# Kernel tuning notes

Measured on AMD Instinct MI355X. Metric: run time of the kernel, lower is better.

## Reference

```python
import jax, jax.numpy as jnp
import numpy as np

V, D, T, B, H, L, FF = 32000, 1024, 1024, 2, 16, 2, 4096


def _ln(x, g, b, eps=1e-5):
    m = x.mean(-1, keepdims=True)
    v = ((x - m) ** 2).mean(-1, keepdims=True)
    return (x - m) * jax.lax.rsqrt(v + eps) * g + b


def setup_inputs() -> dict:
    key = jax.random.key(0)
    ks = jax.random.split(key, 16)
    s = 0.02  # init scale for stable softmax/logits
    return {
        "idx": jax.random.randint(ks[0], (B, T), 0, V),
        "targets": jax.random.randint(ks[1], (B, T), 0, V),
        "word_emb": jax.random.normal(ks[2], (V, D), jnp.float32) * s,
        "pos_emb": jax.random.normal(ks[3], (T, D), jnp.float32) * s,
        "ln1_g": jnp.ones((L, D), jnp.float32),
        "ln1_b": jnp.zeros((L, D), jnp.float32),
        "wq": jax.random.normal(ks[4], (L, D, D), jnp.float32) * s,
        "wk": jax.random.normal(ks[5], (L, D, D), jnp.float32) * s,
        "wv": jax.random.normal(ks[6], (L, D, D), jnp.float32) * s,
        "proj_w": jax.random.normal(ks[7], (L, D, D), jnp.float32) * s,
        "proj_b": jnp.zeros((L, D), jnp.float32),
        "ln2_g": jnp.ones((L, D), jnp.float32),
        "ln2_b": jnp.zeros((L, D), jnp.float32),
        "ff_w1": jax.random.normal(ks[8], (L, D, FF), jnp.float32) * s,
        "ff_b1": jnp.zeros((L, FF), jnp.float32),
        "ff_w2": jax.random.normal(ks[9], (L, FF, D), jnp.float32) * s,
        "ff_b2": jnp.zeros((L, D), jnp.float32),
        "lnf_g": jnp.ones((D,), jnp.float32),
        "lnf_b": jnp.zeros((D,), jnp.float32),
        "lm_w": jax.random.normal(ks[10], (D, V), jnp.float32) * s,
        "lm_b": jnp.zeros((V,), jnp.float32),
    }


def reference(word_emb, pos_emb, ln1_g, ln1_b, wq, wk, wv, proj_w, proj_b,
              ln2_g, ln2_b, ff_w1, ff_b1, ff_w2, ff_b2, lnf_g, lnf_b,
              lm_w, lm_b, idx, targets):
    b, t = idx.shape
    d = word_emb.shape[1]
    n_layer, n_head = wq.shape[0], H
    x = word_emb[idx] + pos_emb[:t]              # [B,T,D]
    causal = jnp.tril(jnp.ones((t, t), bool))
    maps = []
    for l in range(n_layer):
        h = _ln(x, ln1_g[l], ln1_b[l])
        q = (h @ wq[l]).reshape(b, t, n_head, -1)  # [B,T,H,hd]
        k = (h @ wk[l]).reshape(b, t, n_head, -1)
        v = (h @ wv[l]).reshape(b, t, n_head, -1)
        # NOTE: source scales by n_embd**-0.5 (full embedding dim), not head_size
        wei = jnp.einsum('bqhd,bkhd->bhqk', q, k) * (d ** -0.5)
        wei = jnp.where(causal, wei, -jnp.inf)
        wei = jax.nn.softmax(wei, axis=-1)        # [B,H,T,T]
        maps.append(wei)
        att = jnp.einsum('bhqk,bkhd->bqhd', wei, v).reshape(b, t, d)
        x = x + att @ proj_w[l] + proj_b[l]
        h2 = _ln(x, ln2_g[l], ln2_b[l])
        x = x + jax.nn.relu(h2 @ ff_w1[l] + ff_b1[l]) @ ff_w2[l] + ff_b2[l]
    x = _ln(x, lnf_g, lnf_b)
    logits = (x @ lm_w + lm_b).reshape(b * t, -1)  # [B*T, V]
    logp = jax.nn.log_softmax(logits, axis=-1)
    loss = -logp[jnp.arange(b * t), targets.reshape(-1)].mean()
    probs = jax.nn.log_softmax(x, axis=-1)         # source: LogSoftmax of final-LN x
    return (logits, loss, jnp.stack(maps), probs)
```

## Files before the change

### kernel.cpp

```cpp
#include <hip/hip_runtime.h>
#include <hip/hip_bf16.h>

#define VSZ 32000
#define DM  1024
#define TSEQ 1024
#define BB  2
#define HH  16
#define LL  2
#define FFD 4096
#define NTOK (BB*TSEQ)

static constexpr size_t LOGITS_OFF = 0;
static constexpr size_t LOSS_OFF   = (size_t)NTOK * VSZ;
static constexpr size_t MAPS_OFF   = LOSS_OFF + 1;
static constexpr size_t PROBS_OFF  = MAPS_OFF + (size_t)LL*BB*HH*TSEQ*TSEQ;

typedef __attribute__((ext_vector_type(8))) short bf8;
typedef __attribute__((ext_vector_type(4))) float f32x4;
typedef __attribute__((ext_vector_type(4))) short short4v;

__device__ __forceinline__ short f2bf(float f) {
  union { float f; unsigned u; } v; v.f = f;
  unsigned r = v.u + 0x7FFFu + ((v.u >> 16) & 1u);
  return (short)(r >> 16);
}

__device__ __forceinline__ void gload16(const void* g, void* l) {
  __builtin_amdgcn_global_load_lds(
      (const __attribute__((address_space(1))) void*)g,
      (__attribute__((address_space(3))) void*)l, 16, 0, 0);
}

__device__ __forceinline__ float block_sum256(float v, float* sh) {
#pragma unroll
  for (int off = 32; off; off >>= 1) v += __shfl_down(v, off);
  int wid = threadIdx.x >> 6, lane = threadIdx.x & 63;
  if (lane == 0) sh[wid] = v;
  __syncthreads();
  v = sh[0] + sh[1] + sh[2] + sh[3];
  __syncthreads();
  return v;
}
__device__ __forceinline__ float block_max256(float v, float* sh) {
#pragma unroll
  for (int off = 32; off; off >>= 1) v = fmaxf(v, __shfl_down(v, off));
  int wid = threadIdx.x >> 6, lane = threadIdx.x & 63;
  if (lane == 0) sh[wid] = v;
  __syncthreads();
  v = fmaxf(fmaxf(sh[0], sh[1]), fmaxf(sh[2], sh[3]));
  __syncthreads();
  return v;
}

static constexpr size_t PLW = (size_t)4 * DM * DM + (size_t)DM * FFD + (size_t)FFD * DM;
__global__ __launch_bounds__(256) void transpose_all(const float* __restrict__ wq,
    const float* __restrict__ wk, const float* __restrict__ wv,
    const float* __restrict__ proj_w, const float* __restrict__ ff_w1,
    const float* __restrict__ ff_w2, short* __restrict__ wt_base) {
  __shared__ float T[64][65];
  const int bid = blockIdx.x;
  const int l = bid / 3072, r = bid % 3072;
  short* qbase = wt_base + (size_t)l * PLW;
  const float* W; short* Wt; int K, N, tn, tk;
  if (r < 1024) {
    int s = r >> 8, rr = r & 255;
    W = (s == 0 ? wq : (s == 1 ? wk : (s == 2 ? wv : proj_w))) + (size_t)l * DM * DM;
    Wt = qbase + (size_t)s * DM * DM;
    K = DM; N = DM; tn = rr & 15; tk = rr >> 4;
  } else if (r < 2048) {
    int rr = r - 1024;
    W = ff_w1 + (size_t)l * DM * FFD; Wt = qbase + (size_t)4 * DM * DM;
    K = DM; N = FFD; tn = rr & 63; tk = rr >> 6;
  } else {
    int rr = r - 2048;
    W = ff_w2 + (size_t)l * FFD * DM; Wt = qbase + (size_t)4 * DM * DM + (size_t)DM * FFD;
    K = FFD; N = DM; tn = rr & 15; tk = rr >> 4;
  }
  const int n0 = tn * 64, k0 = tk * 64;
  const int tid = threadIdx.x;
  const int lr = tid >> 4, lc4 = (tid & 15) * 4;
#pragma unroll
  for (int p = 0; p < 4; ++p) {
    int k = lr + p * 16;
    float4 w = *(const float4*)&W[(size_t)(k0 + k) * N + n0 + lc4];
    T[k][lc4] = w.x; T[k][lc4+1] = w.y; T[k][lc4+2] = w.z; T[k][lc4+3] = w.w;
  }
  __syncthreads();
#pragma unroll
  for (int p = 0; p < 4; ++p) {
    int n = lr + p * 16;
    short4v s;
    s.x = f2bf(T[lc4  ][n]);
    s.y = f2bf(T[lc4+1][n]);
    s.z = f2bf(T[lc4+2][n]);
    s.w = f2bf(T[lc4+3][n]);
    *(short4v*)&Wt[(size_t)(n0 + n) * K + k0 + lc4] = s;
  }
}

__global__ __launch_bounds__(256) void transpose_cvt(const float* __restrict__ W,
    short* __restrict__ Wt, int K, int N) {
  __shared__ float T[64][65];
  const int n0 = blockIdx.x * 64, k0 = blockIdx.y * 64;
  const int tid = threadIdx.x;
  const int lr = tid >> 4, lc4 = (tid & 15) * 4;
#pragma unroll
  for (int p = 0; p < 4; ++p) {
    int k = lr + p * 16;
    float4 w = *(const float4*)&W[(size_t)(k0 + k) * N + n0 + lc4];
    T[k][lc4] = w.x; T[k][lc4+1] = w.y; T[k][lc4+2] = w.z; T[k][lc4+3] = w.w;
  }
  __syncthreads();
#pragma unroll
  for (int p = 0; p < 4; ++p) {
    int n = lr + p * 16;
    short4v s;
    s.x = f2bf(T[lc4  ][n]);
    s.y = f2bf(T[lc4+1][n]);
    s.z = f2bf(T[lc4+2][n]);
    s.w = f2bf(T[lc4+3][n]);
    *(short4v*)&Wt[(size_t)(n0 + n) * K + k0 + lc4] = s;
  }
}

__global__ __launch_bounds__(256) void embed_kernel(const int* __restrict__ idx,
    const float* __restrict__ we, const float* __restrict__ pe, float* __restrict__ x) {
  int i = blockIdx.x * 256 + threadIdx.x;
  int n = i >> 10;
  int d = i & 1023;
  int t = n & (TSEQ - 1);
  x[i] = we[(size_t)idx[n] * DM + d] + pe[(size_t)t * DM + d];
}

template<int ALSO_F32>
__global__ __launch_bounds__(256) void ln_bf(const float* __restrict__ in,
    const float* __restrict__ g, const float* __restrict__ b,
    short* __restrict__ outb, float* __restrict__ outf) {
  __shared__ float sh[4];
  int row = blockIdx.x, tid = threadIdx.x;
  const float* xr = in + (size_t)row * DM;
  float4 v = *(const float4*)&xr[tid * 4];
  float s  = v.x + v.y + v.z + v.w;
  float s2 = v.x*v.x + v.y*v.y + v.z*v.z + v.w*v.w;
  s  = block_sum256(s, sh);
  s2 = block_sum256(s2, sh);
  float mean = s * (1.0f / DM);
  float var  = s2 * (1.0f / DM) - mean * mean;
  float inv  = rsqrtf(var + 1e-5f);
  float4 gv = *(const float4*)&g[tid * 4];
  float4 bv = *(const float4*)&b[tid * 4];
  float4 o;
  o.x = (v.x - mean) * inv * gv.x + bv.x;
  o.y = (v.y - mean) * inv * gv.y + bv.y;
  o.z = (v.z - mean) * inv * gv.z + bv.z;
  o.w = (v.w - mean) * inv * gv.w + bv.w;
  short4v ob;
  ob.x = f2bf(o.x); ob.y = f2bf(o.y); ob.z = f2bf(o.z); ob.w = f2bf(o.w);
  *(short4v*)&outb[(size_t)row * DM + tid * 4] = ob;
  if (ALSO_F32)
    *(float4*)&outf[(size_t)row * DM + tid * 4] = o;
}

template<int BIAS, int RES, int RELU, int OUTBF>
__global__ __launch_bounds__(256) void gemm_bb(const short* __restrict__ A, int lda,
    const short* __restrict__ Bt, const float* __restrict__ bias,
    void* __restrict__ Cv, int M, int K, int Nn) {
  __shared__ short As[128 * 32];
  __shared__ short Bs[128 * 32];
  float* Cf = (float*)Cv;
  short* Cb = (short*)Cv;
  const int tid  = threadIdx.x;
  const int bm   = blockIdx.x * 128, bn = blockIdx.y * 128;
  const int lane = tid & 63, wid = tid >> 6;
  const int wr = wid >> 1, wc = wid & 1;
  const int lr = lane & 15, lg = lane >> 4;
  const int srow = lane >> 2;
  const int schunk = (lane & 3) * 8;

  f32x4 acc[4][4];
#pragma unroll
  for (int i = 0; i < 4; ++i)
#pragma unroll
    for (int j = 0; j < 4; ++j) acc[i][j] = (f32x4)0.f;

  for (int k0 = 0; k0 < K; k0 += 32) {
#pragma unroll
    for (int t = 0; t < 2; ++t) {
      const int issue = wid * 2 + t;
      const int row = issue * 16 + srow;
      gload16(&A[(size_t)(bm + row) * lda + k0 + schunk], &As[issue * 512]);
      gload16(&Bt[(size_t)(bn + row) * K  + k0 + schunk], &Bs[issue * 512]);
    }
    __syncthreads();
    bf8 af[4], bfv[4];
#pragma unroll
    for (int i = 0; i < 4; ++i)
      af[i] = *(const bf8*)&As[(wr * 64 + i * 16 + lr) * 32 + lg * 8];
#pragma unroll
    for (int j = 0; j < 4; ++j)
      bfv[j] = *(const bf8*)&Bs[(wc * 64 + j * 16 + lr) * 32 + lg * 8];
#pragma unroll
    for (int i = 0; i < 4; ++i)
#pragma unroll
      for (int j = 0; j < 4; ++j)
        acc[i][j] = __builtin_amdgcn_mfma_f32_16x16x32_bf16(af[i], bfv[j], acc[i][j], 0, 0, 0);
    __syncthreads();
  }
#pragma unroll
  for (int i = 0; i < 4; ++i) {
#pragma unroll
    for (int v = 0; v < 4; ++v) {
      int row = bm + wr * 64 + i * 16 + lg * 4 + v;
      size_t rowb = (size_t)row * Nn;
#pragma unroll
      for (int j = 0; j < 4; ++j) {
        int col = bn + wc * 64 + j * 16 + lr;
        float val = acc[i][j][v];
        if (BIAS) val += bias[col];
        if (RES)  val += Cf[rowb + col];
        if (RELU) val = fmaxf(val, 0.f);
        if (OUTBF) Cb[rowb + col] = f2bf(val);
        else       Cf[rowb + col] = val;
      }
    }
  }
}

template<int BIAS>
__global__ __launch_bounds__(256) void gemm_lm_cvt(const float* __restrict__ A,
    const float* __restrict__ Bw, const float* __restrict__ bias,
    float* __restrict__ C, int M, int K, int Nn) {
  __shared__ short As[128 * 40];
  __shared__ short Bs[128 * 40];
  const int tid  = threadIdx.x;
  const int bm   = blockIdx.x * 128, bn = blockIdx.y * 128;
  const int lane = tid & 63, wid = tid >> 6;
  const int wr = wid >> 1, wc = wid & 1;
  const int lr = lane & 15, lg = lane >> 4;
  const int sar = tid >> 3, sak = (tid & 7) * 4;
  const int sbn = tid & 127, sbk = (tid >> 7) * 16;
  f32x4 acc[4][4];
#pragma unroll
  for (int i = 0; i < 4; ++i)
#pragma unroll
    for (int j = 0; j < 4; ++j) acc[i][j] = (f32x4)0.f;
  for (int k0 = 0; k0 < K; k0 += 32) {
#pragma unroll
    for (int p = 0; p < 4; ++p) {
      int row = sar + p * 32;
      float4 a4 = *(const float4*)&A[(size_t)(bm + row) * K + k0 + sak];
      short4v s4;
      s4.x = f2bf(a4.x); s4.y = f2bf(a4.y); s4.z = f2bf(a4.z); s4.w = f2bf(a4.w);
      *(short4v*)&As[row * 40 + sak] = s4;
    }
    {
      short tmp[16];
#pragma unroll
      for (int e = 0; e < 16; ++e)
        tmp[e] = f2bf(Bw[(size_t)(k0 + sbk + e) * Nn + bn + sbn]);
      *(bf8*)&Bs[sbn * 40 + sbk    ] = *(bf8*)&tmp[0];
      *(bf8*)&Bs[sbn * 40 + sbk + 8] = *(bf8*)&tmp[8];
    }
    __syncthreads();
    bf8 af[4], bfv[4];
#pragma unroll
    for (int i = 0; i < 4; ++i)
      af[i] = *(const bf8*)&As[(wr * 64 + i * 16 + lr) * 40 + lg * 8];
#pragma unroll
    for (int j = 0; j < 4; ++j)
      bfv[j] = *(const bf8*)&Bs[(wc * 64 + j * 16 + lr) * 40 + lg * 8];
#pragma unroll
    for (int i = 0; i < 4; ++i)
#pragma unroll
      for (int j = 0; j < 4; ++j)
        acc[i][j] = __builtin_amdgcn_mfma_f32_16x16x32_bf16(af[i], bfv[j], acc[i][j], 0, 0, 0);
    __syncthreads();
  }
#pragma unroll
  for (int i = 0; i < 4; ++i) {
#pragma unroll
    for (int v = 0; v < 4; ++v) {
      int row = bm + wr * 64 + i * 16 + lg * 4 + v;
      size_t rowb = (size_t)row * Nn;
#pragma unroll
      for (int j = 0; j < 4; ++j) {
        int col = bn + wc * 64 + j * 16 + lr;
        float val = acc[i][j][v];
        if (BIAS) val += bias[col];
        C[rowb + col] = val;
      }
    }
  }
}

__global__ __launch_bounds__(256) void attn_qkt(const float* __restrict__ qkv,
    float* __restrict__ maps_l) {
  __shared__ short Qs[64 * 72];
  __shared__ short Ks[64 * 72];
  const int tid = threadIdx.x;
  const int qi = blockIdx.x;
  const int bh = blockIdx.y;
  const int b = bh >> 4, h = bh & 15;
  const int q0 = qi * 64;
  const int lane = tid & 63, wid = tid >> 6;
  const int wr = wid >> 1, wc = wid & 1;
  const int lr = lane & 15, lg = lane >> 4;
  const int sr = tid >> 2, sc = (tid & 3) * 16;
  {
    const float* src = &qkv[(size_t)(b * TSEQ + q0 + sr) * 3072 + h * 64 + sc];
    short tmp[16];
#pragma unroll
    for (int e = 0; e < 16; ++e) tmp[e] = f2bf(src[e]);
    *(bf8*)&Qs[sr * 72 + sc    ] = *(bf8*)&tmp[0];
    *(bf8*)&Qs[sr * 72 + sc + 8] = *(bf8*)&tmp[8];
  }
  float* mbase = maps_l + (size_t)bh * TSEQ * TSEQ;
  for (int kt = 0; kt <= qi; ++kt) {
    const int k0 = kt * 64;
    {
      const float* src = &qkv[(size_t)(b * TSEQ + k0 + sr) * 3072 + 1024 + h * 64 + sc];
      short tmp[16];
#pragma unroll
      for (int e = 0; e < 16; ++e) tmp[e] = f2bf(src[e]);
      *(bf8*)&Ks[sr * 72 + sc    ] = *(bf8*)&tmp[0];
      *(bf8*)&Ks[sr * 72 + sc + 8] = *(bf8*)&tmp[8];
    }
    __syncthreads();
    f32x4 acc[2][2];
#pragma unroll
    for (int i = 0; i < 2; ++i)
#pragma unroll
      for (int j = 0; j < 2; ++j) acc[i][j] = (f32x4)0.f;
#pragma unroll
    for (int ds = 0; ds < 2; ++ds) {
      bf8 af[2], bfv[2];
#pragma unroll
      for (int i = 0; i < 2; ++i)
        af[i] = *(const bf8*)&Qs[(wr * 32 + i * 16 + lr) * 72 + ds * 32 + lg * 8];
#pragma unroll
      for (int j = 0; j < 2; ++j)
        bfv[j] = *(const bf8*)&Ks[(wc * 32 + j * 16 + lr) * 72 + ds * 32 + lg * 8];
#pragma unroll
      for (int i = 0; i < 2; ++i)
#pragma unroll
        for (int j = 0; j < 2; ++j)
          acc[i][j] = __builtin_amdgcn_mfma_f32_16x16x32_bf16(af[i], bfv[j], acc[i][j], 0, 0, 0);
    }
#pragma unroll
    for (int i = 0; i < 2; ++i)
#pragma unroll
      for (int v = 0; v < 4; ++v) {
        int row = q0 + wr * 32 + i * 16 + lg * 4 + v;
#pragma unroll
        for (int j = 0; j < 2; ++j) {
          int col = k0 + wc * 32 + j * 16 + lr;
          mbase[(size_t)row * TSEQ + col] = acc[i][j][v] * 0.03125f;
        }
      }
    __syncthreads();
  }
}

__global__ __launch_bounds__(256) void attn_softmax(float* __restrict__ maps_l) {
  __shared__ float sh[4];
  const int q = blockIdx.x, bh = blockIdx.y;
  const int tid = threadIdx.x;
  float* mrow = maps_l + (size_t)bh * TSEQ * TSEQ + (size_t)q * TSEQ;
  float s[4];
#pragma unroll
  for (int i = 0; i < 4; ++i) {
    int kp = tid + i * 256;
    s[i] = (kp <= q) ? mrow[kp] : -1e30f;
  }
  float m = block_max256(fmaxf(fmaxf(s[0], s[1]), fmaxf(s[2], s[3])), sh);
  float e[4]; float ssum = 0.f;
#pragma unroll
  for (int i = 0; i < 4; ++i) {
    int kp = tid + i * 256;
    e[i] = (kp <= q) ? __expf(s[i] - m) : 0.f;
    ssum += e[i];
  }
  ssum = block_sum256(ssum, sh);
  float inv = 1.f / ssum;
#pragma unroll
  for (int i = 0; i < 4; ++i) mrow[tid + i * 256] = e[i] * inv;
}

__global__ __launch_bounds__(256) void attn_av2(const float* __restrict__ maps_l,
    const float* __restrict__ qkv, short* __restrict__ att_bf) {
  __shared__ float Vs[64][68];
  __shared__ float Ws[32][66];
  const int tid = threadIdx.x;
  const int ql = tid >> 3, dg = tid & 7;
  const int q0 = blockIdx.x * 32;
  const int bh = blockIdx.y;
  const int b = bh >> 4, h = bh & 15;
  const float* wbase = maps_l + (size_t)bh * TSEQ * TSEQ;
  const int vr = tid >> 2, vc = (tid & 3) * 16;
  const int wrow = tid >> 3, wc8 = (tid & 7) * 8;
  float4 a0 = {0,0,0,0}, a1 = {0,0,0,0};
  const int ntiles = (q0 + 32 + 63) >> 6;
  for (int kt = 0; kt < ntiles; ++kt) {
    const int kb0 = kt * 64;
#pragma unroll
    for (int e = 0; e < 4; ++e)
      *(float4*)&Vs[vr][vc + e * 4] =
        *(const float4*)&qkv[(size_t)(b * TSEQ + kb0 + vr) * 3072 + 2048 + h * 64 + vc + e * 4];
#pragma unroll
    for (int e = 0; e < 4; ++e)
      *(float2*)&Ws[wrow][wc8 + e * 2] =
        *(const float2*)&wbase[(size_t)(q0 + wrow) * TSEQ + kb0 + wc8 + e * 2];
    __syncthreads();
#pragma unroll 8
    for (int k = 0; k < 64; ++k) {
      float w = Ws[ql][k];
      float4 v0 = *(const float4*)&Vs[k][dg * 8];
      float4 v1 = *(const float4*)&Vs[k][dg * 8 + 4];
      a0.x += w * v0.x; a0.y += w * v0.y; a0.z += w * v0.z; a0.w += w * v0.w;
      a1.x += w * v1.x; a1.y += w * v1.y; a1.z += w * v1.z; a1.w += w * v1.w;
    }
    __syncthreads();
  }
  short* orow = &att_bf[(size_t)(b * TSEQ + q0 + ql) * DM + h * 64 + dg * 8];
  short4v s0, s1;
  s0.x = f2bf(a0.x); s0.y = f2bf(a0.y); s0.z = f2bf(a0.z); s0.w = f2bf(a0.w);
  s1.x = f2bf(a1.x); s1.y = f2bf(a1.y); s1.z = f2bf(a1.z); s1.w = f2bf(a1.w);
  *(short4v*)&orow[0] = s0;
  *(short4v*)&orow[4] = s1;
}

__global__ __launch_bounds__(256) void loss_rows(const float* __restrict__ logits,
    const int* __restrict__ targets, float* __restrict__ rowloss) {
  __shared__ float sh[4];
  int row = blockIdx.x, tid = threadIdx.x;
  const float* lr = logits + (size_t)row * VSZ;
  float m = -1e30f;
  for (int i = tid; i < VSZ; i += 256) m = fmaxf(m, lr[i]);
  m = block_max256(m, sh);
  float ssum = 0.f;
  for (int i = tid; i < VSZ; i += 256) ssum += __expf(lr[i] - m);
  ssum = block_sum256(ssum, sh);
  if (tid == 0)
    rowloss[row] = m + logf(ssum) - lr[targets[row]];
}
__global__ __launch_bounds__(256) void loss_reduce(const float* __restrict__ rowloss,
    float* __restrict__ out) {
  __shared__ float sh[4];
  float s = 0.f;
  for (int i = threadIdx.x; i < NTOK; i += 256) s += rowloss[i];
  s = block_sum256(s, sh);
  if (threadIdx.x == 0) out[0] = s * (1.0f / NTOK);
}
__global__ __launch_bounds__(256) void probs_rows(const float* __restrict__ xf,
    float* __restrict__ out) {
  __shared__ float sh[4];
  int row = blockIdx.x, tid = threadIdx.x;
  const float* xr = xf + (size_t)row * DM;
  float4 v = *(const float4*)&xr[tid * 4];
  float m = block_max256(fmaxf(fmaxf(v.x, v.y), fmaxf(v.z, v.w)), sh);
  float ssum = __expf(v.x-m) + __expf(v.y-m) + __expf(v.z-m) + __expf(v.w-m);
  ssum = block_sum256(ssum, sh);
  float lg = m + logf(ssum);
  float* orow = out + (size_t)row * DM + tid * 4;
  orow[0] = v.x - lg;
  orow[1] = v.y - lg;
  orow[2] = v.z - lg;
  orow[3] = v.w - lg;
}

extern "C" void kernel_launch(void* const* d_in, const int* in_sizes, int n_in,
                              void* d_out, int out_size, void* d_ws, size_t ws_size,
                              hipStream_t stream) {
  const int*   idx      = (const int*)  d_in[0];
  const int*   targets  = (const int*)  d_in[1];
  const float* word_emb = (const float*)d_in[2];
  const float* pos_emb  = (const float*)d_in[3];
  const float* ln1_g    = (const float*)d_in[4];
  const float* ln1_b    = (const float*)d_in[5];
  const float* wq       = (const float*)d_in[6];
  const float* wk       = (const float*)d_in[7];
  const float* wv       = (const float*)d_in[8];
  const float* proj_w   = (const float*)d_in[9];
  const float* proj_b   = (const float*)d_in[10];
  const float* ln2_g    = (const float*)d_in[11];
  const float* ln2_b    = (const float*)d_in[12];
  const float* ff_w1    = (const float*)d_in[13];
  const float* ff_b1    = (const float*)d_in[14];
  const float* ff_w2    = (const float*)d_in[15];
  const float* ff_b2    = (const float*)d_in[16];
  const float* lnf_g    = (const float*)d_in[17];
  const float* lnf_b    = (const float*)d_in[18];
  const float* lm_w     = (const float*)d_in[19];
  const float* lm_b     = (const float*)d_in[20];

  float* outf   = (float*)d_out;
  float* logits = outf + LOGITS_OFF;
  float* lossp  = outf + LOSS_OFF;
  float* maps   = outf + MAPS_OFF;
  float* probs  = outf + PROBS_OFF;

  const size_t ND = (size_t)NTOK * DM;
  float* x    = (float*)d_ws;
  float* xf   = x + ND;
  float* qkvb = xf + ND;
  float* rowloss = qkvb + (size_t)NTOK * 3072;
  short* h_bf   = (short*)(rowloss + NTOK);
  short* att_bf = h_bf + ND;
  short* ffh_bf = att_bf + ND;
  short* xf_bf  = ffh_bf + (size_t)NTOK * FFD;
  char*  ws_end = (char*)(xf_bf + ND);
  const size_t act_bytes = (size_t)(ws_end - (char*)d_ws);
  const size_t lmwt_bytes = (size_t)VSZ * DM * sizeof(short);
  const int lm_fast = (ws_size >= act_bytes + lmwt_bytes);
  short* lm_wt = (short*)ws_end;

  short* wt_base = (short*)logits;
  auto layer_wt = [&](int l) { return wt_base + (size_t)l * PLW; };

  dim3 b256(256);
  transpose_all<<<dim3(2 * 3072), b256, 0, stream>>>(wq, wk, wv, proj_w, ff_w1, ff_w2, wt_base);
  if (lm_fast)
    transpose_cvt<<<dim3(VSZ/64, 16), b256, 0, stream>>>(lm_w, lm_wt, DM, VSZ);

  embed_kernel<<<dim3((NTOK * DM) / 256), b256, 0, stream>>>(idx, word_emb, pos_emb, x);

  for (int l = 0; l < LL; ++l) {
    short* qkvt = layer_wt(l);
    short* projt = qkvt + (size_t)3 * DM * DM;
    short* ff1t  = projt + (size_t)DM * DM;
    short* ff2t  = ff1t + (size_t)DM * FFD;
    ln_bf<0><<<dim3(NTOK), b256, 0, stream>>>(x, ln1_g + l * DM, ln1_b + l * DM, h_bf, nullptr);
    gemm_bb<0,0,0,0><<<dim3(NTOK/128, 3072/128), b256, 0, stream>>>(h_bf, DM, qkvt, nullptr, qkvb, NTOK, DM, 3072);
    float* maps_l = maps + (size_t)l * BB * HH * TSEQ * TSEQ;
    attn_qkt<<<dim3(TSEQ/64, BB*HH), b256, 0, stream>>>(qkvb, maps_l);
    attn_softmax<<<dim3(TSEQ, BB*HH), b256, 0, stream>>>(maps_l);
    attn_av2<<<dim3(TSEQ/32, BB*HH), b256, 0, stream>>>(maps_l, qkvb, att_bf);
    gemm_bb<1,1,0,0><<<dim3(NTOK/128, DM/128), b256, 0, stream>>>(att_bf, DM, projt, proj_b + l * DM, x, NTOK, DM, DM);
    ln_bf<0><<<dim3(NTOK), b256, 0, stream>>>(x, ln2_g + l * DM, ln2_b + l * DM, h_bf, nullptr);
    gemm_bb<1,0,1,1><<<dim3(NTOK/128, FFD/128), b256, 0, stream>>>(h_bf, DM, ff1t, ff_b1 + l * FFD, ffh_bf, NTOK, DM, FFD);
    gemm_bb<1,1,0,0><<<dim3(NTOK/128, DM/128), b256, 0, stream>>>(ffh_bf, FFD, ff2t, ff_b2 + l * DM, x, NTOK, FFD, DM);
  }

  ln_bf<1><<<dim3(NTOK), b256, 0, stream>>>(x, lnf_g, lnf_b, xf_bf, xf);
  if (lm_fast)
    gemm_bb<1,0,0,0><<<dim3(NTOK/128, VSZ/128), b256, 0, stream>>>(xf_bf, DM, lm_wt, lm_b, logits, NTOK, DM, VSZ);
  else
    gemm_lm_cvt<1><<<dim3(NTOK/128, VSZ/128), b256, 0, stream>>>(xf, lm_w, lm_b, logits, NTOK, DM, VSZ);
  loss_rows<<<dim3(NTOK), b256, 0, stream>>>(logits, targets, rowloss);
  loss_reduce<<<dim3(1), b256, 0, stream>>>(rowloss, lossp);
  probs_rows<<<dim3(NTOK), b256, 0, stream>>>(xf, probs);

  (void)in_sizes; (void)n_in; (void)out_size;
}
```

Measured before the change: 1.220 ms.

## Fuse QK^T with causal softmax in LDS and store QKV as bf16

Merges the QK^T score kernel and the row-softmax kernel into one kernel. It keeps a 16-query strip of scores in shared memory, so the maps buffer is written once instead of written, read and rewritten. The QKV GEMM now writes bf16 output, which halves QKV traffic, and the attention kernels read bf16 directly. V is converted back to fp32 in LDS for the AV step. The upper-triangle zeros are now written explicitly. The cost is a large LDS footprint (about 66KB per block), which limits occupancy, and only 16 query rows per block for the MFMA work.

After: 1.216 ms. About the same (-0.3%).

```diff
diff --git a/kernel.cpp b/kernel.cpp
--- a/kernel.cpp
+++ b/kernel.cpp
@@ -9,6 +9,7 @@
 #define LL  2
 #define FFD 4096
 #define NTOK (BB*TSEQ)
+#define QT  16
 
 static constexpr size_t LOGITS_OFF = 0;
 static constexpr size_t LOSS_OFF   = (size_t)NTOK * VSZ;
@@ -23,6 +24,10 @@
   union { float f; unsigned u; } v; v.f = f;
   unsigned r = v.u + 0x7FFFu + ((v.u >> 16) & 1u);
   return (short)(r >> 16);
+}
+__device__ __forceinline__ float bf2f(short s) {
+  union { unsigned u; float f; } v; v.u = ((unsigned)(unsigned short)s) << 16;
+  return v.f;
 }
 
 __device__ __forceinline__ void gload16(const void* g, void* l) {
@@ -293,101 +298,62 @@
   }
 }
 
-__global__ __launch_bounds__(256) void attn_qkt(const float* __restrict__ qkv,
+__global__ __launch_bounds__(256) void attn_fused(const short* __restrict__ qkv_bf,
     float* __restrict__ maps_l) {
-  __shared__ short Qs[64 * 72];
+  __shared__ float S[QT][1032];
+  __shared__ short Qs[QT * 72];
   __shared__ short Ks[64 * 72];
   const int tid = threadIdx.x;
-  const int qi = blockIdx.x;
+  const int q0 = blockIdx.x * QT;
   const int bh = blockIdx.y;
   const int b = bh >> 4, h = bh & 15;
-  const int q0 = qi * 64;
   const int lane = tid & 63, wid = tid >> 6;
-  const int wr = wid >> 1, wc = wid & 1;
   const int lr = lane & 15, lg = lane >> 4;
-  const int sr = tid >> 2, sc = (tid & 3) * 16;
-  {
-    const float* src = &qkv[(size_t)(b * TSEQ + q0 + sr) * 3072 + h * 64 + sc];
-    short tmp[16];
-#pragma unroll
-    for (int e = 0; e < 16; ++e) tmp[e] = f2bf(src[e]);
-    *(bf8*)&Qs[sr * 72 + sc    ] = *(bf8*)&tmp[0];
-    *(bf8*)&Qs[sr * 72 + sc + 8] = *(bf8*)&tmp[8];
-  }
-  float* mbase = maps_l + (size_t)bh * TSEQ * TSEQ;
-  for (int kt = 0; kt <= qi; ++kt) {
+  if (tid < 128) {
+    int r = tid >> 3, c8 = (tid & 7) * 8;
+    *(bf8*)&Qs[r * 72 + c8] =
+      *(const bf8*)&qkv_bf[(size_t)(b * TSEQ + q0 + r) * 3072 + h * 64 + c8];
+  }
+  const int ktmax = (q0 + QT - 1) / 64 + 1;
+  for (int kt = 0; kt < ktmax; ++kt) {
     const int k0 = kt * 64;
     {
-      const float* src = &qkv[(size_t)(b * TSEQ + k0 + sr) * 3072 + 1024 + h * 64 + sc];
-      short tmp[16];
-#pragma unroll
-      for (int e = 0; e < 16; ++e) tmp[e] = f2bf(src[e]);
-      *(bf8*)&Ks[sr * 72 + sc    ] = *(bf8*)&tmp[0];
-      *(bf8*)&Ks[sr * 72 + sc + 8] = *(bf8*)&tmp[8];
-    }
-    __syncthreads();
-    f32x4 acc[2][2];
-#pragma unroll
-    for (int i = 0; i < 2; ++i)
-#pragma unroll
-      for (int j = 0; j < 2; ++j) acc[i][j] = (f32x4)0.f;
+      int r = tid >> 2, c16 = (tid & 3) * 16;
+      const short* src = &qkv_bf[(size_t)(b * TSEQ + k0 + r) * 3072 + 1024 + h * 64 + c16];
+      *(bf8*)&Ks[r * 72 + c16    ] = *(const bf8*)&src[0];
+      *(bf8*)&Ks[r * 72 + c16 + 8] = *(const bf8*)&src[8];
+    }
+    __syncthreads();
+    f32x4 acc = (f32x4)0.f;
 #pragma unroll
     for (int ds = 0; ds < 2; ++ds) {
-      bf8 af[2], bfv[2];
-#pragma unroll
-      for (int i = 0; i < 2; ++i)
-        af[i] = *(const bf8*)&Qs[(wr * 32 + i * 16 + lr) * 72 + ds * 32 + lg * 8];
-#pragma unroll
-      for (int j = 0; j < 2; ++j)
-        bfv[j] = *(const bf8*)&Ks[(wc * 32 + j * 16 + lr) * 72 + ds * 32 + lg * 8];
-#pragma unroll
-      for (int i = 0; i < 2; ++i)
-#pragma unroll
-        for (int j = 0; j < 2; ++j)
-          acc[i][j] = __builtin_amdgcn_mfma_f32_16x16x32_bf16(af[i], bfv[j], acc[i][j], 0, 0, 0);
-    }
-#pragma unroll
-    for (int i = 0; i < 2; ++i)
-#pragma unroll
-      for (int v = 0; v < 4; ++v) {
-        int row = q0 + wr * 32 + i * 16 + lg * 4 + v;
-#pragma unroll
-        for (int j = 0; j < 2; ++j) {
-          int col = k0 + wc * 32 + j * 16 + lr;
-          mbase[(size_t)row * TSEQ + col] = acc[i][j][v] * 0.03125f;
-        }
-      }
-    __syncthreads();
-  }
-}
-
-__global__ __launch_bounds__(256) void attn_softmax(float* __restrict__ maps_l) {
-  __shared__ float sh[4];
-  const int q = blockIdx.x, bh = blockIdx.y;
-  const int tid = threadIdx.x;
-  float* mrow = maps_l + (size_t)bh * TSEQ * TSEQ + (size_t)q * TSEQ;
-  float s[4];
-#pragma unroll
-  for (int i = 0; i < 4; ++i) {
-    int kp = tid + i * 256;
-    s[i] = (kp <= q) ? mrow[kp] : -1e30f;
-  }
-  float m = block_max256(fmaxf(fmaxf(s[0], s[1]), fmaxf(s[2], s[3])), sh);
-  float e[4]; float ssum = 0.f;
-#pragma unroll
-  for (int i = 0; i < 4; ++i) {
-    int kp = tid + i * 256;
-    e[i] = (kp <= q) ? __expf(s[i] - m) : 0.f;
-    ssum += e[i];
-  }
-  ssum = block_sum256(ssum, sh);
-  float inv = 1.f / ssum;
-#pragma unroll
-  for (int i = 0; i < 4; ++i) mrow[tid + i * 256] = e[i] * inv;
+      bf8 af  = *(const bf8*)&Qs[lr * 72 + ds * 32 + lg * 8];
+      bf8 bfv = *(const bf8*)&Ks[(wid * 16 + lr) * 72 + ds * 32 + lg * 8];
+      acc = __builtin_amdgcn_mfma_f32_16x16x32_bf16(af, bfv, acc, 0, 0, 0);
+    }
+#pragma unroll
+    for (int v = 0; v < 4; ++v)
+      S[lg * 4 + v][k0 + wid * 16 + lr] = acc[v] * 0.03125f;
+    __syncthreads();
+  }
+  const int r = tid >> 4, l16 = tid & 15;
+  const int qg = q0 + r;
+  float m = -1e30f;
+  for (int c = l16; c <= qg; c += 16) m = fmaxf(m, S[r][c]);
+#pragma unroll
+  for (int off = 8; off; off >>= 1) m = fmaxf(m, __shfl_xor(m, off, 16));
+  float ssum = 0.f;
+  for (int c = l16; c <= qg; c += 16) ssum += __expf(S[r][c] - m);
+#pragma unroll
+  for (int off = 8; off; off >>= 1) ssum += __shfl_xor(ssum, off, 16);
+  const float inv = 1.f / ssum;
+  float* mrow = maps_l + (size_t)bh * TSEQ * TSEQ + (size_t)qg * TSEQ;
+  for (int c = l16; c < TSEQ; c += 16)
+    mrow[c] = (c <= qg) ? __expf(S[r][c] - m) * inv : 0.f;
 }
 
 __global__ __launch_bounds__(256) void attn_av2(const float* __restrict__ maps_l,
-    const float* __restrict__ qkv, short* __restrict__ att_bf) {
+    const short* __restrict__ qkv_bf, short* __restrict__ att_bf) {
   __shared__ float Vs[64][68];
   __shared__ float Ws[32][66];
   const int tid = threadIdx.x;
@@ -402,10 +368,15 @@
   const int ntiles = (q0 + 32 + 63) >> 6;
   for (int kt = 0; kt < ntiles; ++kt) {
     const int kb0 = kt * 64;
-#pragma unroll
-    for (int e = 0; e < 4; ++e)
-      *(float4*)&Vs[vr][vc + e * 4] =
-        *(const float4*)&qkv[(size_t)(b * TSEQ + kb0 + vr) * 3072 + 2048 + h * 64 + vc + e * 4];
+    {
+      const short* src = &qkv_bf[(size_t)(b * TSEQ + kb0 + vr) * 3072 + 2048 + h * 64 + vc];
+      bf8 v0 = *(const bf8*)&src[0];
+      bf8 v1 = *(const bf8*)&src[8];
+#pragma unroll
+      for (int e = 0; e < 8; ++e) Vs[vr][vc + e]     = bf2f(v0[e]);
+#pragma unroll
+      for (int e = 0; e < 8; ++e) Vs[vr][vc + 8 + e] = bf2f(v1[e]);
+    }
 #pragma unroll
     for (int e = 0; e < 4; ++e)
       *(float2*)&Ws[wrow][wc8 + e * 2] =
@@ -502,9 +473,9 @@
   const size_t ND = (size_t)NTOK * DM;
   float* x    = (float*)d_ws;
   float* xf   = x + ND;
-  float* qkvb = xf + ND;
-  float* rowloss = qkvb + (size_t)NTOK * 3072;
-  short* h_bf   = (short*)(rowloss + NTOK);
+  float* rowloss = xf + ND;
+  short* qkv_bf = (short*)(rowloss + NTOK);
+  short* h_bf   = qkv_bf + 3 * ND;
   short* att_bf = h_bf + ND;
   short* ffh_bf = att_bf + ND;
   short* xf_bf  = ffh_bf + (size_t)NTOK * FFD;
@@ -530,11 +501,10 @@
     short* ff1t  = projt + (size_t)DM * DM;
     short* ff2t  = ff1t + (size_t)DM * FFD;
     ln_bf<0><<<dim3(NTOK), b256, 0, stream>>>(x, ln1_g + l * DM, ln1_b + l * DM, h_bf, nullptr);
-    gemm_bb<0,0,0,0><<<dim3(NTOK/128, 3072/128), b256, 0, stream>>>(h_bf, DM, qkvt, nullptr, qkvb, NTOK, DM, 3072);
+    gemm_bb<0,0,0,1><<<dim3(NTOK/128, 3072/128), b256, 0, stream>>>(h_bf, DM, qkvt, nullptr, qkv_bf, NTOK, DM, 3072);
     float* maps_l = maps + (size_t)l * BB * HH * TSEQ * TSEQ;
-    attn_qkt<<<dim3(TSEQ/64, BB*HH), b256, 0, stream>>>(qkvb, maps_l);
-    attn_softmax<<<dim3(TSEQ, BB*HH), b256, 0, stream>>>(maps_l);
-    attn_av2<<<dim3(TSEQ/32, BB*HH), b256, 0, stream>>>(maps_l, qkvb, att_bf);
+    attn_fused<<<dim3(TSEQ/QT, BB*HH), b256, 0, stream>>>(qkv_bf, maps_l);
+    attn_av2<<<dim3(TSEQ/32, BB*HH), b256, 0, stream>>>(maps_l, qkv_bf, att_bf);
     gemm_bb<1,1,0,0><<<dim3(NTOK/128, DM/128), b256, 0, stream>>>(att_bf, DM, projt, proj_b + l * DM, x, NTOK, DM, DM);
     ln_bf<0><<<dim3(NTOK), b256, 0, stream>>>(x, ln2_g + l * DM, ln2_b + l * DM, h_bf, nullptr);
     gemm_bb<1,0,1,1><<<dim3(NTOK/128, FFD/128), b256, 0, stream>>>(h_bf, DM, ff1t, ff_b1 + l * FFD, ffh_bf, NTOK, DM, FFD);
```
